# Kernel tuning notes

Hardware: AMD Instinct MI355X
Metric: run time of the kernel (lower is better)

The kernel has to match this reference:

```python
import jax, jax.numpy as jnp
import numpy as np


def setup_inputs() -> dict:
    key = jax.random.key(0)
    k1, k2, k3 = jax.random.split(key, 3)
    B, IN, EXP, K = 1024, 1024, 40, 7
    OUT = IN * EXP  # 40960
    x = jax.random.normal(k1, (B, IN), dtype=jnp.float32)
    # fixed fan-in projection matrix: K nonzeros per output row
    vals = jax.random.uniform(k2, (OUT, K), dtype=jnp.float32)
    idx = jax.random.randint(k3, (OUT, K), 0, IN, dtype=jnp.int32)
    return {"x": x, "vals": vals, "idx": idx}


def reference(x, vals, idx):
    # y[b, o] = sum_k vals[o, k] * x[b, idx[o, k]]
    # equivalent to (W_sparse @ x.T).T with W in COO, fixed fan-in K.
    # Loop over the small fixed fan-in K (=7) to avoid a [B, OUT, K] intermediate.
    K = idx.shape[1]
    y = x[:, idx[:, 0]] * vals[:, 0][None, :]  # [B, OUT]
    for k in range(1, K):
        y = y + x[:, idx[:, k]] * vals[:, k][None, :]
    return y
```

## Files before the change

kernel.cpp:

```cpp
#include <hip/hip_runtime.h>
#include <hip/hip_fp16.h>

#define BATCH   1024
#define IN      1024
#define OUT     40960
#define KF      7
#define BT      8
#define NO      4
#define THREADS 256
#define OTILE   (THREADS * NO)
#define CHUNKS  (OUT / 64)

#define PMETA_BYTES ((size_t)CHUNKS * KF * 64 * 8)
#define XPK_BYTES   ((size_t)(BATCH / 8) * IN * 8 * 2)


__global__ __launch_bounds__(THREADS)
void repack_kernel(const float* __restrict__ x, const float* __restrict__ vals,
                   const int* __restrict__ idx,
                   uint2* __restrict__ pmeta, __half* __restrict__ xpk)
{
    const int gid = blockIdx.x * THREADS + threadIdx.x;
    if (blockIdx.x < 512) {
        const int g = gid >> 10;
        const int i = gid & 1023;
        const float* xb = x + (size_t)g * 8 * IN + i;
        union { __half h[8]; float4 f; } u;
#pragma unroll
        for (int r = 0; r < 8; ++r) u.h[r] = __float2half_rn(xb[(size_t)r * IN]);
        *(float4*)&xpk[(size_t)gid * 8] = u.f;
    } else {
        const int t2 = gid - 512 * THREADS;
        const int c  = t2 / (KF * 64);
        const int r  = t2 % (KF * 64);
        const int k  = r >> 6;
        const int l  = r & 63;
        const size_t src = (size_t)(c * 64 + l) * KF + k;
        uint2 m;
        m.x = (unsigned)(idx[src] << 4);
        m.y = __float_as_uint(vals[src]);
        pmeta[t2] = m;
    }
}

__global__ __launch_bounds__(THREADS, 8)
void sparse_proj(const uint2* __restrict__ pmeta, const __half* __restrict__ xpk,
                 float* __restrict__ y)
{
    __shared__ __align__(16) __half xs[IN * 8];

    const int t     = threadIdx.x;
    const int b0    = blockIdx.y * BT;
    const int obase = blockIdx.x * OTILE + t;

    {
        const float4* src = (const float4*)(xpk + (size_t)blockIdx.y * IN * 8);
        float4* dst = (float4*)xs;
#pragma unroll
        for (int r = 0; r < 4; ++r) dst[t + r * THREADS] = src[t + r * THREADS];
    }
    __syncthreads();

    const int w    = t >> 6;
    const int lane = t & 63;

    const uint2* mbase = pmeta + (size_t)(blockIdx.x * 16 + w) * (KF * 64) + lane;

#pragma unroll
    for (int no = 0; no < NO; ++no) {
        uint2 mc[KF];
#pragma unroll
        for (int k = 0; k < KF; ++k)
            mc[k] = mbase[(size_t)no * 4 * (KF * 64) + k * 64];

        float acc[BT];
#pragma unroll
        for (int r = 0; r < BT; ++r) acc[r] = 0.0f;

#pragma unroll
        for (int k = 0; k < KF; ++k) {
            const unsigned off = mc[k].x;
            const float v = __uint_as_float(mc[k].y);
            const float4 g0 = *(const float4*)((const char*)xs + off);
            const __half2 a0 = *(const __half2*)&g0.x;
            const __half2 a1 = *(const __half2*)&g0.y;
            const __half2 a2 = *(const __half2*)&g0.z;
            const __half2 a3 = *(const __half2*)&g0.w;
            acc[0] = fmaf(v, __low2float(a0),  acc[0]);
            acc[1] = fmaf(v, __high2float(a0), acc[1]);
            acc[2] = fmaf(v, __low2float(a1),  acc[2]);
            acc[3] = fmaf(v, __high2float(a1), acc[3]);
            acc[4] = fmaf(v, __low2float(a2),  acc[4]);
            acc[5] = fmaf(v, __high2float(a2), acc[5]);
            acc[6] = fmaf(v, __low2float(a3),  acc[6]);
            acc[7] = fmaf(v, __high2float(a3), acc[7]);
        }

        const int o = obase + no * THREADS;
#pragma unroll
        for (int r = 0; r < BT; ++r) {
            y[(size_t)(b0 + r) * OUT + o] = acc[r];
        }
    }
}

extern "C" void kernel_launch(void* const* d_in, const int* in_sizes, int n_in,
                              void* d_out, int out_size, void* d_ws, size_t ws_size,
                              hipStream_t stream) {
    const float* x    = (const float*)d_in[0];
    const float* vals = (const float*)d_in[1];
    const int*   idx  = (const int*)d_in[2];
    float*       y    = (float*)d_out;

    uint2*  pmeta = (uint2*)d_ws;
    __half* xpk   = (__half*)((char*)d_ws + PMETA_BYTES);

    repack_kernel<<<dim3(512 + 1120), dim3(THREADS), 0, stream>>>(
        x, vals, idx, pmeta, xpk);

    dim3 grid(OUT / OTILE, BATCH / BT);
    sparse_proj<<<grid, dim3(THREADS), 0, stream>>>(pmeta, xpk, y);
}
```

Baseline: 175.0 us.

## Give each thread four contiguous outputs with vectorized metadata loads and float4 stores

Changes the metadata layout so each thread owns four adjacent outputs per 256-output chunk. Per fan-in step it reads their index/value pairs with two uint4 loads, prefetching the next step. Outputs are written as float4 stores instead of scalar stores, to cut global memory instruction count for the dominant output write. Keeping 32 accumulators per thread raises register pressure, so the launch-bounds occupancy hint drops from 8 to 5.

```diff
diff --git a/kernel.cpp b/kernel.cpp
--- a/kernel.cpp
+++ b/kernel.cpp
@@ -6,12 +6,10 @@
 #define OUT     40960
 #define KF      7
 #define BT      8
-#define NO      4
 #define THREADS 256
-#define OTILE   (THREADS * NO)
-#define CHUNKS  (OUT / 64)
+#define OTILE   1024
 
-#define PMETA_BYTES ((size_t)CHUNKS * KF * 64 * 8)
+#define PMETA_BYTES ((size_t)OUT * KF * 8)
 #define XPK_BYTES   ((size_t)(BATCH / 8) * IN * 8 * 2)
 
 
@@ -30,12 +28,13 @@
         for (int r = 0; r < 8; ++r) u.h[r] = __float2half_rn(xb[(size_t)r * IN]);
         *(float4*)&xpk[(size_t)gid * 8] = u.f;
     } else {
-        const int t2 = gid - 512 * THREADS;
-        const int c  = t2 / (KF * 64);
-        const int r  = t2 % (KF * 64);
-        const int k  = r >> 6;
-        const int l  = r & 63;
-        const size_t src = (size_t)(c * 64 + l) * KF + k;
+        const int t2   = gid - 512 * THREADS;
+        const int c256 = t2 / (KF * 256);
+        const int rem  = t2 % (KF * 256);
+        const int k    = rem >> 8;
+        const int l4   = rem & 255;
+        const int o    = c256 * 256 + l4;
+        const size_t src = (size_t)o * KF + k;
         uint2 m;
         m.x = (unsigned)(idx[src] << 4);
         m.y = __float_as_uint(vals[src]);
@@ -43,15 +42,14 @@
     }
 }
 
-__global__ __launch_bounds__(THREADS, 8)
+__global__ __launch_bounds__(THREADS, 5)
 void sparse_proj(const uint2* __restrict__ pmeta, const __half* __restrict__ xpk,
                  float* __restrict__ y)
 {
     __shared__ __align__(16) __half xs[IN * 8];
 
-    const int t     = threadIdx.x;
-    const int b0    = blockIdx.y * BT;
-    const int obase = blockIdx.x * OTILE + t;
+    const int t  = threadIdx.x;
+    const int b0 = blockIdx.y * BT;
 
     {
         const float4* src = (const float4*)(xpk + (size_t)blockIdx.y * IN * 8);
@@ -63,44 +61,56 @@
 
     const int w    = t >> 6;
     const int lane = t & 63;
+    const int c256 = blockIdx.x * 4 + w;
 
-    const uint2* mbase = pmeta + (size_t)(blockIdx.x * 16 + w) * (KF * 64) + lane;
+    const uint4* mb4 = (const uint4*)pmeta + (size_t)c256 * KF * 128 + lane * 2;
+
+    float acc[4][BT];
+#pragma unroll
+    for (int j = 0; j < 4; ++j)
+#pragma unroll
+        for (int r = 0; r < BT; ++r) acc[j][r] = 0.0f;
+
+    uint4 q0 = mb4[0], q1 = mb4[1];
+#pragma unroll
+    for (int k = 0; k < KF; ++k) {
+        uint4 n0, n1;
+        if (k + 1 < KF) { n0 = mb4[(k + 1) * 128]; n1 = mb4[(k + 1) * 128 + 1]; }
+
+        const unsigned off0 = q0.x, off1 = q0.z, off2 = q1.x, off3 = q1.z;
+        const float v0 = __uint_as_float(q0.y);
+        const float v1 = __uint_as_float(q0.w);
+        const float v2 = __uint_as_float(q1.y);
+        const float v3 = __uint_as_float(q1.w);
 
 #pragma unroll
-    for (int no = 0; no < NO; ++no) {
-        uint2 mc[KF];
+        for (int j = 0; j < 4; ++j) {
+            const unsigned off = (j == 0) ? off0 : (j == 1) ? off1
+                               : (j == 2) ? off2 : off3;
+            const float v = (j == 0) ? v0 : (j == 1) ? v1 : (j == 2) ? v2 : v3;
+            const float4 g = *(const float4*)((const char*)xs + off);
+            const __half2 a0 = *(const __half2*)&g.x;
+            const __half2 a1 = *(const __half2*)&g.y;
+            const __half2 a2 = *(const __half2*)&g.z;
+            const __half2 a3 = *(const __half2*)&g.w;
+            acc[j][0] = fmaf(v, __low2float(a0),  acc[j][0]);
+            acc[j][1] = fmaf(v, __high2float(a0), acc[j][1]);
+            acc[j][2] = fmaf(v, __low2float(a1),  acc[j][2]);
+            acc[j][3] = fmaf(v, __high2float(a1), acc[j][3]);
+            acc[j][4] = fmaf(v, __low2float(a2),  acc[j][4]);
+            acc[j][5] = fmaf(v, __high2float(a2), acc[j][5]);
+            acc[j][6] = fmaf(v, __low2float(a3),  acc[j][6]);
+            acc[j][7] = fmaf(v, __high2float(a3), acc[j][7]);
+        }
+        q0 = n0; q1 = n1;
+    }
+
+    const int o0 = blockIdx.x * OTILE + w * 256 + lane * 4;
 #pragma unroll
-        for (int k = 0; k < KF; ++k)
-            mc[k] = mbase[(size_t)no * 4 * (KF * 64) + k * 64];
-
-        float acc[BT];
-#pragma unroll
-        for (int r = 0; r < BT; ++r) acc[r] = 0.0f;
-
-#pragma unroll
-        for (int k = 0; k < KF; ++k) {
-            const unsigned off = mc[k].x;
-            const float v = __uint_as_float(mc[k].y);
-            const float4 g0 = *(const float4*)((const char*)xs + off);
-            const __half2 a0 = *(const __half2*)&g0.x;
-            const __half2 a1 = *(const __half2*)&g0.y;
-            const __half2 a2 = *(const __half2*)&g0.z;
-            const __half2 a3 = *(const __half2*)&g0.w;
-            acc[0] = fmaf(v, __low2float(a0),  acc[0]);
-            acc[1] = fmaf(v, __high2float(a0), acc[1]);
-            acc[2] = fmaf(v, __low2float(a1),  acc[2]);
-            acc[3] = fmaf(v, __high2float(a1), acc[3]);
-            acc[4] = fmaf(v, __low2float(a2),  acc[4]);
-            acc[5] = fmaf(v, __high2float(a2), acc[5]);
-            acc[6] = fmaf(v, __low2float(a3),  acc[6]);
-            acc[7] = fmaf(v, __high2float(a3), acc[7]);
-        }
-
-        const int o = obase + no * THREADS;
-#pragma unroll
-        for (int r = 0; r < BT; ++r) {
-            y[(size_t)(b0 + r) * OUT + o] = acc[r];
-        }
+    for (int r = 0; r < BT; ++r) {
+        float4 f;
+        f.x = acc[0][r]; f.y = acc[1][r]; f.z = acc[2][r]; f.w = acc[3][r];
+        *(float4*)&y[(size_t)(b0 + r) * OUT + o0] = f;
     }
 }
 
```

Measured after the change: 575.9 us. 3.29x slower.
